# Kernel tuning notes

Hardware: AMD Instinct MI355X
Metric: run time of the kernel (lower is better)

Reference implementation:

```python
import jax, jax.numpy as jnp
import numpy as np

K = 3          # kernel_size
N = K * K      # sampling points per pixel
STRIDE = 1
PAD = 1
DIL = 1


def _conv2d(x, w, b):
    # standard NCHW conv for offset / modulation branches
    y = jax.lax.conv_general_dilated(
        x, w, window_strides=(STRIDE, STRIDE),
        padding=((PAD, PAD), (PAD, PAD)),
        rhs_dilation=(DIL, DIL),
        dimension_numbers=('NCHW', 'OIHW', 'NCHW'))
    return y + b[None, :, None, None]


def setup_inputs() -> dict:
    key = jax.random.key(0)
    ks = jax.random.split(key, 6)
    B, C, H, W, O = 8, 64, 96, 96, 64
    x = jax.random.normal(ks[0], (B, C, H, W), jnp.float32)
    # small random offset/modulation weights so sampling points are off-grid
    offset_w = jax.random.normal(ks[1], (2 * N, C, K, K), jnp.float32) * 0.01
    offset_b = jax.random.normal(ks[2], (2 * N,), jnp.float32) * 0.1
    m_w = jax.random.normal(ks[3], (N, C, K, K), jnp.float32) * 0.01
    m_b = jnp.zeros((N,), jnp.float32)
    # Conv3d(in=C, out=O, kernel=(1,1,N)) weight squeezed to [O, C, N]
    conv_w = jax.random.normal(ks[4], (O, C, N), jnp.float32) * (2.0 / (C * N)) ** 0.5
    conv_b = jnp.zeros((O,), jnp.float32)
    return dict(x=x, offset_w=offset_w, offset_b=offset_b,
                m_w=m_w, m_b=m_b, conv_w=conv_w, conv_b=conv_b)


def _deform_forward(x, offset_w, offset_b, m_w, m_b, conv_w, conv_b):
    B, C, H, W = x.shape
    offset = _conv2d(x, offset_w, offset_b)           # [B, 2n, h, w]
    m = jax.nn.sigmoid(_conv2d(x, m_w, m_b))          # [B, n, h, w]
    xp = jnp.pad(x, ((0, 0), (0, 0), (PAD, PAD), (PAD, PAD)))
    Hp, Wp = xp.shape[2], xp.shape[3]
    off = jnp.transpose(offset, (0, 2, 3, 1))         # [B, h, w, 2n]
    mod = jnp.transpose(m, (0, 2, 3, 1))              # [B, h, w, n]

    # p0: conv-center grid on the padded input; pn: kernel-tap offsets
    st = ((K - 1) // 2) * DIL
    p0_x = jnp.arange(st, Hp - (K // 2) * DIL, STRIDE, dtype=jnp.float32)  # [h]
    p0_y = jnp.arange(st, Wp - (K // 2) * DIL, STRIDE, dtype=jnp.float32)  # [w]
    r = jnp.arange(-((K - 1) // 2) * DIL, (K // 2) * DIL + 1, DIL, dtype=jnp.float32)
    pn_x, pn_y = jnp.meshgrid(r, r, indexing='ij')
    pn_x, pn_y = pn_x.reshape(N), pn_y.reshape(N)

    p_x = off[..., :N] + p0_x[None, :, None, None] + pn_x  # [B, h, w, n]
    p_y = off[..., N:] + p0_y[None, None, :, None] + pn_y

    fl_x = jnp.floor(jax.lax.stop_gradient(p_x))
    fl_y = jnp.floor(jax.lax.stop_gradient(p_y))
    q_tl_x = jnp.clip(fl_x, 0, Hp - 1).astype(jnp.int32)
    q_tl_y = jnp.clip(fl_y, 0, Wp - 1).astype(jnp.int32)
    q_br_x = jnp.clip(fl_x + 1, 0, Hp - 1).astype(jnp.int32)
    q_br_y = jnp.clip(fl_y + 1, 0, Wp - 1).astype(jnp.int32)

    pcx = jnp.clip(p_x, 0, Hp - 1)
    pcy = jnp.clip(p_y, 0, Wp - 1)

    tlx = q_tl_x.astype(pcx.dtype); tly = q_tl_y.astype(pcy.dtype)
    brx = q_br_x.astype(pcx.dtype); bry = q_br_y.astype(pcy.dtype)
    g_tl = (1 + (tlx - pcx)) * (1 + (tly - pcy))
    g_tr = (1 + (tlx - pcx)) * (1 - (bry - pcy))
    g_bl = (1 - (brx - pcx)) * (1 + (tly - pcy))
    g_br = (1 - (brx - pcx)) * (1 - (bry - pcy))

    xflat = xp.reshape(B, C, Hp * Wp)

    def gather(qx, qy):
        # per-batch gather: xf [C, Hp*Wp], idx [h, w, n] -> [C, h, w, n]
        return jax.vmap(lambda xf, i: xf[:, i])(xflat, qx * Wp + qy)

    xq_tl = gather(q_tl_x, q_tl_y)
    xq_tr = gather(q_tl_x, q_br_y)
    xq_bl = gather(q_br_x, q_tl_y)
    xq_br = gather(q_br_x, q_br_y)

    x_p = (g_tl[:, None] * xq_tl + g_tr[:, None] * xq_tr +
           g_bl[:, None] * xq_bl + g_br[:, None] * xq_br)
    x_p = x_p * mod[:, None]                           # modulation

    # Conv3d with (1,1,N) kernel == contraction over (C, N)
    out = jnp.einsum('bchwn,ocn->bohw', x_p, conv_w) + conv_b[None, :, None, None]
    return out


def reference(x, offset_w, offset_b, m_w, m_b, conv_w, conv_b):
    return _deform_forward(x, offset_w, offset_b, m_w, m_b, conv_w, conv_b)
```

## Files before the change

kernel.cpp:

```cpp
#include <hip/hip_runtime.h>
#include <hip/hip_fp16.h>
#include <cstddef>

#define B_   8
#define H_   96
#define W_   96
#define HW_  9216
#define PIX_ 73728

#define NWR    7
#define NWC    38
#define WINPX  266
#define NSLOTS 19

typedef __attribute__((ext_vector_type(8))) _Float16 halfx8;
typedef __attribute__((ext_vector_type(2))) __fp16 fp16x2_raw;
typedef __attribute__((ext_vector_type(4))) float floatx4;

#define XT_OFF   0
#define WFM_OFF  (XT_OFF + PIX_*64*2)
#define WFO_OFF  (WFM_OFF + 18*4*64*8*2)
#define WZ_OFF   (WFO_OFF + 18*2*64*8*2)

__device__ __forceinline__ unsigned pk2h(float a, float b) {
    fp16x2_raw h = __builtin_amdgcn_cvt_pkrtz(a, b);
    union { fp16x2_raw h2; unsigned u; } t; t.h2 = h; return t.u;
}
__device__ __forceinline__ halfx8 uph8(uint4 u) {
    union { uint4 u4; halfx8 h; } t; t.u4 = u; return t.h;
}
__device__ __forceinline__ halfx8 splat8(unsigned d) {
    union { unsigned u[4]; halfx8 h; } t;
    t.u[0] = d; t.u[1] = d; t.u[2] = d; t.u[3] = d; return t.h;
}
__device__ __forceinline__ void async_ld16(const void* g, void* l) {
    __builtin_amdgcn_global_load_lds((const __attribute__((address_space(1))) void*)g,
                                     (__attribute__((address_space(3))) void*)l,
                                     16, 0, 0);
}

__global__ __launch_bounds__(256) void k_transpose(const float* __restrict__ x,
                                                   unsigned short* __restrict__ xt,
                                                   const float* __restrict__ offw,
                                                   const float* __restrict__ mw,
                                                   const float* __restrict__ convw,
                                                   unsigned short* __restrict__ wfm,
                                                   unsigned short* __restrict__ wfo,
                                                   unsigned short* __restrict__ wz) {
    if (blockIdx.x >= 1152) {
        int g = (blockIdx.x - 1152) * 256 + threadIdx.x;
        if (g < 4608) {
            int lane = g & 63, mtks = g >> 6;
            int mt = mtks & 3, ks = mtks >> 2;
            int o = mt * 16 + (lane & 15), quad = lane >> 4;
            float v[8];
            #pragma unroll
            for (int j = 0; j < 8; ++j) {
                int k = ks * 32 + quad * 8 + j;
                int t = k / 64, c = k % 64;
                v[j] = convw[(size_t)(o * 64 + c) * 9 + t];
            }
            uint4 pk;
            pk.x = pk2h(v[0], v[1]); pk.y = pk2h(v[2], v[3]);
            pk.z = pk2h(v[4], v[5]); pk.w = pk2h(v[6], v[7]);
            *(uint4*)(wfm + (size_t)g * 8) = pk;
        } else if (g < 4608 + 2304) {
            int g2 = g - 4608;
            int lane = g2 & 63, mtks = g2 >> 6;
            int mt = mtks & 1, ks = mtks >> 1;
            int m = mt * 16 + (lane & 15), quad = lane >> 4;
            float v[8];
            #pragma unroll
            for (int j = 0; j < 8; ++j) {
                int k = ks * 32 + quad * 8 + j;
                int t = k / 64, c = k % 64;
                float f = 0.f;
                if (m < 18)      f = offw[(size_t)(m * 64 + c) * 9 + t];
                else if (m < 27) f = mw[(size_t)((m - 18) * 64 + c) * 9 + t];
                v[j] = f;
            }
            uint4 pk;
            pk.x = pk2h(v[0], v[1]); pk.y = pk2h(v[2], v[3]);
            pk.z = pk2h(v[4], v[5]); pk.w = pk2h(v[6], v[7]);
            *(uint4*)(wfo + (size_t)g2 * 8) = pk;
        } else if (g < 4608 + 2304 + 8) {
            uint4 z = make_uint4(0, 0, 0, 0);
            *(uint4*)(wz + (size_t)(g - 6912) * 8) = z;
        }
        return;
    }

    __shared__ float tile[64 * 65];
    int bb  = blockIdx.x / 144;
    int sp0 = (blockIdx.x % 144) * 64;
    int t = threadIdx.x;
    int s4 = (t & 15) * 4, cq = t >> 4;
    #pragma unroll
    for (int i = 0; i < 4; ++i) {
        int c = cq + 16 * i;
        float4 v = *(const float4*)&x[(size_t)(bb * 64 + c) * HW_ + sp0 + s4];
        tile[c * 65 + s4 + 0] = v.x;
        tile[c * 65 + s4 + 1] = v.y;
        tile[c * 65 + s4 + 2] = v.z;
        tile[c * 65 + s4 + 3] = v.w;
    }
    __syncthreads();
    int c8 = t & 7, sgrp = t >> 3;
    #pragma unroll
    for (int i = 0; i < 2; ++i) {
        int s2 = i * 32 + sgrp;
        uint4 pk;
        pk.x = pk2h(tile[(c8 * 8 + 0) * 65 + s2], tile[(c8 * 8 + 1) * 65 + s2]);
        pk.y = pk2h(tile[(c8 * 8 + 2) * 65 + s2], tile[(c8 * 8 + 3) * 65 + s2]);
        pk.z = pk2h(tile[(c8 * 8 + 4) * 65 + s2], tile[(c8 * 8 + 5) * 65 + s2]);
        pk.w = pk2h(tile[(c8 * 8 + 6) * 65 + s2], tile[(c8 * 8 + 7) * 65 + s2]);
        *(uint4*)(xt + (size_t)(bb * HW_ + sp0 + s2) * 64 + c8 * 8) = pk;
    }
}

__global__ __launch_bounds__(384, 4) void k_fused(const unsigned short* __restrict__ xt,
                                                  const unsigned short* __restrict__ wfo,
                                                  const unsigned short* __restrict__ wfm,
                                                  const float* __restrict__ offb,
                                                  const float* __restrict__ mb,
                                                  const float* __restrict__ convb,
                                                  const unsigned short* __restrict__ wz,
                                                  float* __restrict__ out) {
    __shared__ __align__(16) unsigned char s_win[(WINPX + NSLOTS) * 128];
    __shared__ __align__(16) unsigned char s_u[96 * 9 * 16];
    __shared__ int s_cnt;
    float* s_off = (float*)s_u;
    unsigned char* s_meta = s_u;

    int tid = threadIdx.x;
    int w = tid >> 6, lane = tid & 63, col = lane & 15, quad = lane >> 4;
    int blk = (blockIdx.x & 7) * 96 + (blockIdx.x >> 3);
    int bb  = blk / 96;
    int rem = blk % 96;
    int hr  = (rem / 3) * 3;
    int wc  = (rem % 3) * 32;
    const unsigned short* xtb = xt + (size_t)bb * HW_ * 64;

    if (tid == 0) s_cnt = 0;
    {
        int p0  = lane >> 3;
        int cgx = (lane & 7) ^ p0;
        const unsigned short* wzp = wz + cgx * 8;
        for (int i = w; i < 34; i += 6) {
            int p = i * 8 + p0;
            int wr = p / NWC, wcl = p - wr * NWC;
            int gr = hr - 2 + wr, gc = wc - 3 + wcl;
            bool ok = (p < WINPX) && ((unsigned)gr < 96u) && ((unsigned)gc < 96u);
            const unsigned short* src = ok ? (xtb + ((size_t)(gr * 96 + gc) * 64 + cgx * 8)) : wzp;
            async_ld16(src, s_win + i * 1024);
        }
    }
    __syncthreads();

    floatx4 aoff0 = (floatx4){0.f, 0.f, 0.f, 0.f};
    floatx4 aoff1 = (floatx4){0.f, 0.f, 0.f, 0.f};
    {
        int wr_base = 2 + (w >> 1);
        int wc_base = 3 + (w & 1) * 16 + col;
        #pragma unroll
        for (int t = 0; t < 9; ++t) {
            int dh = t / 3 - 1, dw = t % 3 - 1;
            int p = (wr_base + dh) * NWC + (wc_base + dw);
            int pb = p << 7, psw = (p & 7) << 4;
            #pragma unroll
            for (int ksl = 0; ksl < 2; ++ksl) {
                int ks = t * 2 + ksl;
                halfx8 a0 = *(const halfx8*)(wfo + ((size_t)(ks * 2 + 0) * 64 + lane) * 8);
                halfx8 a1 = *(const halfx8*)(wfo + ((size_t)(ks * 2 + 1) * 64 + lane) * 8);
                uint4 bvu = *(const uint4*)(s_win + pb + ((quad * 16 + ksl * 64) ^ psw));
                halfx8 bv = uph8(bvu);
                aoff0 = __builtin_amdgcn_mfma_f32_16x16x32_f16(a0, bv, aoff0, 0, 0, 0);
                aoff1 = __builtin_amdgcn_mfma_f32_16x16x32_f16(a1, bv, aoff1, 0, 0, 0);
            }
        }
    }
    #pragma unroll
    for (int r = 0; r < 4; ++r) {
        s_off[(quad * 4 + r) * 98 + (w * 16 + col)] = aoff0[r];
        int m = 16 + quad * 4 + r;
        if (m < 27) s_off[m * 98 + (w * 16 + col)] = aoff1[r];
    }
    __syncthreads();

    float ox0, oy0, mv0, ox1, oy1, mv1, ox2 = 0.f, oy2 = 0.f, mv2 = 0.f;
    bool has2 = tid < 96;
    {
        int px = tid % 96, n = tid / 96;
        ox0 = s_off[n * 98 + px]        + offb[n];
        oy0 = s_off[(9 + n) * 98 + px]  + offb[9 + n];
        mv0 = s_off[(18 + n) * 98 + px] + mb[n];
    }
    {
        int id = tid + 384;
        int px = id % 96, n = id / 96;
        ox1 = s_off[n * 98 + px]        + offb[n];
        oy1 = s_off[(9 + n) * 98 + px]  + offb[9 + n];
        mv1 = s_off[(18 + n) * 98 + px] + mb[n];
    }
    if (has2) {
        int id = tid + 768;
        int px = id % 96, n = id / 96;
        ox2 = s_off[n * 98 + px]        + offb[n];
        oy2 = s_off[(9 + n) * 98 + px]  + offb[9 + n];
        mv2 = s_off[(18 + n) * 98 + px] + mb[n];
    }
    __syncthreads();

    auto meta_one = [&](int id, float ox, float oy, float mv) {
        int px = id % 96, n = id / 96;
        float modv = 1.f / (1.f + __expf(-mv));
        int prow = hr + (px >> 5), pcol = wc + (px & 31);
        float pxx = ox + (float)(prow + 1) + (float)(n / 3 - 1);
        float pyy = oy + (float)(pcol + 1) + (float)(n % 3 - 1);
        float flx = floorf(pxx), fly = floorf(pyy);
        float tlxf = fminf(fmaxf(flx,       0.f), 97.f);
        float tlyf = fminf(fmaxf(fly,       0.f), 97.f);
        float brxf = fminf(fmaxf(flx + 1.f, 0.f), 97.f);
        float bryf = fminf(fmaxf(fly + 1.f, 0.f), 97.f);
        float pcx  = fminf(fmaxf(pxx, 0.f), 97.f);
        float pcy  = fminf(fmaxf(pyy, 0.f), 97.f);
        float gx0 = 1.f + tlxf - pcx;
        float gx1 = 1.f - (brxf - pcx);
        float gy0 = 1.f + tlyf - pcy;
        float gy1 = 1.f - (bryf - pcy);
        int tlx = (int)tlxf, tly = (int)tlyf, brx = (int)brxf, bry = (int)bryf;
        int   qxs[4] = {tlx, tlx, brx, brx};
        int   qys[4] = {tly, bry, tly, bry};
        float gs4[4] = {gx0 * gy0, gx0 * gy1, gx1 * gy0, gx1 * gy1};
        unsigned short si[4]; unsigned short hg[4];
        #pragma unroll
        for (int c4 = 0; c4 < 4; ++c4) {
            int qx = qxs[c4], qy = qys[c4];
            bool valid = (qx >= 1) && (qx <= 96) && (qy >= 1) && (qy <= 96);
            int gr = qx - 1, gc = qy - 1;
            int wr = gr - (hr - 2), wcl = gc - (wc - 3);
            bool inwin = ((unsigned)wr < (unsigned)NWR) && ((unsigned)wcl < (unsigned)NWC);
            unsigned short idxv; float gvf;
            if (inwin) {
                idxv = (unsigned short)(wr * NWC + wcl);
                gvf = gs4[c4] * modv;
            } else if (!valid) {
                idxv = 0; gvf = 0.f;
            } else {
                int s = atomicAdd(&s_cnt, 1);
                int gidx = gr * 96 + gc;
                if (s < NSLOTS) {
                    int ps = WINPX + s;
                    #pragma unroll
                    for (int ch = 0; ch < 8; ++ch) {
                        uint4 v = *(const uint4*)(xtb + (size_t)gidx * 64 + ch * 8);
                        *(uint4*)(s_win + (size_t)ps * 128 + ((ch ^ (ps & 7)) * 16)) = v;
                    }
                    idxv = (unsigned short)ps;
                } else {
                    idxv = (unsigned short)(0x8000u | (unsigned)gidx);
                }
                gvf = gs4[c4] * modv;
            }
            si[c4] = idxv;
            hg[c4] = __half_as_ushort(__float2half_rn(gvf));
        }
        uint4 mw4;
        mw4.x = si[0] | ((unsigned)si[1] << 16);
        mw4.y = si[2] | ((unsigned)si[3] << 16);
        mw4.z = hg[0] | ((unsigned)hg[1] << 16);
        mw4.w = hg[2] | ((unsigned)hg[3] << 16);
        *(uint4*)(s_meta + ((size_t)px * 9 + n) * 16) = mw4;
    };
    meta_one(tid,       ox0, oy0, mv0);
    meta_one(tid + 384, ox1, oy1, mv1);
    if (has2) meta_one(tid + 768, ox2, oy2, mv2);
    __syncthreads();

    int px3 = w * 16 + col;
    floatx4 acc[4];
    #pragma unroll
    for (int mt = 0; mt < 4; ++mt) acc[mt] = (floatx4){0.f, 0.f, 0.f, 0.f};

    int qk0 = quad * 16, qk1 = quad * 16 + 64;

    #pragma unroll
    for (int n = 0; n < 9; ++n) {
        uint4 mu = *(const uint4*)(s_meta + ((size_t)px3 * 9 + n) * 16);
        unsigned i0 = mu.x & 0xFFFFu, i1 = mu.x >> 16;
        unsigned i2 = mu.y & 0xFFFFu, i3 = mu.y >> 16;
        int pm0 = (i0 & 0x8000u) ? 0 : (int)i0;
        int pm1 = (i1 & 0x8000u) ? 0 : (int)i1;
        int pm2 = (i2 & 0x8000u) ? 0 : (int)i2;
        int pm3 = (i3 & 0x8000u) ? 0 : (int)i3;
        int b0 = pm0 << 7, s0 = (pm0 & 7) << 4;
        int b1 = pm1 << 7, s1 = (pm1 & 7) << 4;
        int b2 = pm2 << 7, s2 = (pm2 & 7) << 4;
        int b3 = pm3 << 7, s3 = (pm3 & 7) << 4;
        uint4 cA0 = *(const uint4*)(s_win + b0 + (qk0 ^ s0));
        uint4 cA1 = *(const uint4*)(s_win + b1 + (qk0 ^ s1));
        uint4 cA2 = *(const uint4*)(s_win + b2 + (qk0 ^ s2));
        uint4 cA3 = *(const uint4*)(s_win + b3 + (qk0 ^ s3));
        uint4 cB0 = *(const uint4*)(s_win + b0 + (qk1 ^ s0));
        uint4 cB1 = *(const uint4*)(s_win + b1 + (qk1 ^ s1));
        uint4 cB2 = *(const uint4*)(s_win + b2 + (qk1 ^ s2));
        uint4 cB3 = *(const uint4*)(s_win + b3 + (qk1 ^ s3));
        if (__any((int)((i0 | i1 | i2 | i3) & 0x8000u))) {
            if (i0 & 0x8000u) { size_t ga = (size_t)(i0 & 0x3FFFu) * 64 + quad * 8;
                cA0 = *(const uint4*)(xtb + ga); cB0 = *(const uint4*)(xtb + ga + 32); }
            if (i1 & 0x8000u) { size_t ga = (size_t)(i1 & 0x3FFFu) * 64 + quad * 8;
                cA1 = *(const uint4*)(xtb + ga); cB1 = *(const uint4*)(xtb + ga + 32); }
            if (i2 & 0x8000u) { size_t ga = (size_t)(i2 & 0x3FFFu) * 64 + quad * 8;
                cA2 = *(const uint4*)(xtb + ga); cB2 = *(const uint4*)(xtb + ga + 32); }
            if (i3 & 0x8000u) { size_t ga = (size_t)(i3 & 0x3FFFu) * 64 + quad * 8;
                cA3 = *(const uint4*)(xtb + ga); cB3 = *(const uint4*)(xtb + ga + 32); }
        }
        unsigned gl0 = (mu.z & 0xFFFFu) | (mu.z << 16);
        unsigned gl1 = (mu.z >> 16) | (mu.z & 0xFFFF0000u);
        unsigned gl2 = (mu.w & 0xFFFFu) | (mu.w << 16);
        unsigned gl3 = (mu.w >> 16) | (mu.w & 0xFFFF0000u);
        halfx8 g0 = splat8(gl0), g1 = splat8(gl1), g2 = splat8(gl2), g3 = splat8(gl3);
        halfx8 vA = uph8(cA0) * g0;
        vA += uph8(cA1) * g1; vA += uph8(cA2) * g2; vA += uph8(cA3) * g3;
        halfx8 vB = uph8(cB0) * g0;
        vB += uph8(cB1) * g1; vB += uph8(cB2) * g2; vB += uph8(cB3) * g3;
        #pragma unroll
        for (int mt = 0; mt < 4; ++mt) {
            halfx8 afA = *(const halfx8*)(wfm + ((size_t)((n * 2 + 0) * 4 + mt) * 64 + lane) * 8);
            halfx8 afB = *(const halfx8*)(wfm + ((size_t)((n * 2 + 1) * 4 + mt) * 64 + lane) * 8);
            acc[mt] = __builtin_amdgcn_mfma_f32_16x16x32_f16(afA, vA, acc[mt], 0, 0, 0);
            acc[mt] = __builtin_amdgcn_mfma_f32_16x16x32_f16(afB, vB, acc[mt], 0, 0, 0);
        }
    }

    int sp = (hr + (w >> 1)) * 96 + wc + (w & 1) * 16 + col;
    #pragma unroll
    for (int mt = 0; mt < 4; ++mt) {
        float4 cb4 = *(const float4*)&convb[mt * 16 + quad * 4];
        #pragma unroll
        for (int r = 0; r < 4; ++r) {
            int o = mt * 16 + quad * 4 + r;
            float bias = (r == 0) ? cb4.x : (r == 1) ? cb4.y : (r == 2) ? cb4.z : cb4.w;
            out[(size_t)(bb * 64 + o) * HW_ + sp] = acc[mt][r] + bias;
        }
    }
}

extern "C" void kernel_launch(void* const* d_in, const int* in_sizes, int n_in,
                              void* d_out, int out_size, void* d_ws, size_t ws_size,
                              hipStream_t stream) {
    const float* x     = (const float*)d_in[0];
    const float* offw  = (const float*)d_in[1];
    const float* offb  = (const float*)d_in[2];
    const float* mw    = (const float*)d_in[3];
    const float* mb    = (const float*)d_in[4];
    const float* convw = (const float*)d_in[5];
    const float* convb = (const float*)d_in[6];
    char* ws = (char*)d_ws;
    unsigned short* xt16 = (unsigned short*)(ws + XT_OFF);
    unsigned short* wfm  = (unsigned short*)(ws + WFM_OFF);
    unsigned short* wfo  = (unsigned short*)(ws + WFO_OFF);
    unsigned short* wz   = (unsigned short*)(ws + WZ_OFF);
    float* out = (float*)d_out;

    k_transpose<<<dim3(1152 + 28), dim3(256), 0, stream>>>(x, xt16, offw, mw, convw, wfm, wfo, wz);
    k_fused    <<<dim3(768),       dim3(384), 0, stream>>>(xt16, wfo, wfm, offb, mb, convb, wz, out);
}
```

Measured before the change: 109.3 us.

## Fuse transpose and deform kernels into one cooperative launch with grid sync

```diff
diff --git a/kernel.cpp b/kernel.cpp
--- a/kernel.cpp
+++ b/kernel.cpp
@@ -1,6 +1,9 @@
 #include <hip/hip_runtime.h>
 #include <hip/hip_fp16.h>
+#include <hip/hip_cooperative_groups.h>
 #include <cstddef>
+
+namespace cg = cooperative_groups;
 
 #define B_   8
 #define H_   96
@@ -39,109 +42,64 @@
                                      16, 0, 0);
 }
 
-__global__ __launch_bounds__(256) void k_transpose(const float* __restrict__ x,
-                                                   unsigned short* __restrict__ xt,
-                                                   const float* __restrict__ offw,
-                                                   const float* __restrict__ mw,
-                                                   const float* __restrict__ convw,
-                                                   unsigned short* __restrict__ wfm,
-                                                   unsigned short* __restrict__ wfo,
-                                                   unsigned short* __restrict__ wz) {
-    if (blockIdx.x >= 1152) {
-        int g = (blockIdx.x - 1152) * 256 + threadIdx.x;
-        if (g < 4608) {
-            int lane = g & 63, mtks = g >> 6;
-            int mt = mtks & 3, ks = mtks >> 2;
-            int o = mt * 16 + (lane & 15), quad = lane >> 4;
-            float v[8];
-            #pragma unroll
-            for (int j = 0; j < 8; ++j) {
-                int k = ks * 32 + quad * 8 + j;
-                int t = k / 64, c = k % 64;
-                v[j] = convw[(size_t)(o * 64 + c) * 9 + t];
-            }
-            uint4 pk;
-            pk.x = pk2h(v[0], v[1]); pk.y = pk2h(v[2], v[3]);
-            pk.z = pk2h(v[4], v[5]); pk.w = pk2h(v[6], v[7]);
-            *(uint4*)(wfm + (size_t)g * 8) = pk;
-        } else if (g < 4608 + 2304) {
-            int g2 = g - 4608;
-            int lane = g2 & 63, mtks = g2 >> 6;
-            int mt = mtks & 1, ks = mtks >> 1;
-            int m = mt * 16 + (lane & 15), quad = lane >> 4;
-            float v[8];
-            #pragma unroll
-            for (int j = 0; j < 8; ++j) {
-                int k = ks * 32 + quad * 8 + j;
-                int t = k / 64, c = k % 64;
-                float f = 0.f;
-                if (m < 18)      f = offw[(size_t)(m * 64 + c) * 9 + t];
-                else if (m < 27) f = mw[(size_t)((m - 18) * 64 + c) * 9 + t];
-                v[j] = f;
-            }
-            uint4 pk;
-            pk.x = pk2h(v[0], v[1]); pk.y = pk2h(v[2], v[3]);
-            pk.z = pk2h(v[4], v[5]); pk.w = pk2h(v[6], v[7]);
-            *(uint4*)(wfo + (size_t)g2 * 8) = pk;
-        } else if (g < 4608 + 2304 + 8) {
-            uint4 z = make_uint4(0, 0, 0, 0);
-            *(uint4*)(wz + (size_t)(g - 6912) * 8) = z;
-        }
-        return;
-    }
-
-    __shared__ float tile[64 * 65];
-    int bb  = blockIdx.x / 144;
-    int sp0 = (blockIdx.x % 144) * 64;
-    int t = threadIdx.x;
-    int s4 = (t & 15) * 4, cq = t >> 4;
-    #pragma unroll
-    for (int i = 0; i < 4; ++i) {
-        int c = cq + 16 * i;
-        float4 v = *(const float4*)&x[(size_t)(bb * 64 + c) * HW_ + sp0 + s4];
-        tile[c * 65 + s4 + 0] = v.x;
-        tile[c * 65 + s4 + 1] = v.y;
-        tile[c * 65 + s4 + 2] = v.z;
-        tile[c * 65 + s4 + 3] = v.w;
-    }
-    __syncthreads();
-    int c8 = t & 7, sgrp = t >> 3;
-    #pragma unroll
-    for (int i = 0; i < 2; ++i) {
-        int s2 = i * 32 + sgrp;
+__device__ __forceinline__ void prep_weight_item(int g,
+                                                 const float* __restrict__ offw,
+                                                 const float* __restrict__ mw,
+                                                 const float* __restrict__ convw,
+                                                 unsigned short* __restrict__ wfm,
+                                                 unsigned short* __restrict__ wfo) {
+    if (g < 4608) {
+        int lane = g & 63, mtks = g >> 6;
+        int mt = mtks & 3, ks = mtks >> 2;
+        int o = mt * 16 + (lane & 15), quad = lane >> 4;
+        float v[8];
+        #pragma unroll
+        for (int j = 0; j < 8; ++j) {
+            int k = ks * 32 + quad * 8 + j;
+            int t = k / 64, c = k % 64;
+            v[j] = convw[(size_t)(o * 64 + c) * 9 + t];
+        }
         uint4 pk;
-        pk.x = pk2h(tile[(c8 * 8 + 0) * 65 + s2], tile[(c8 * 8 + 1) * 65 + s2]);
-        pk.y = pk2h(tile[(c8 * 8 + 2) * 65 + s2], tile[(c8 * 8 + 3) * 65 + s2]);
-        pk.z = pk2h(tile[(c8 * 8 + 4) * 65 + s2], tile[(c8 * 8 + 5) * 65 + s2]);
-        pk.w = pk2h(tile[(c8 * 8 + 6) * 65 + s2], tile[(c8 * 8 + 7) * 65 + s2]);
-        *(uint4*)(xt + (size_t)(bb * HW_ + sp0 + s2) * 64 + c8 * 8) = pk;
-    }
-}
-
-__global__ __launch_bounds__(384, 4) void k_fused(const unsigned short* __restrict__ xt,
-                                                  const unsigned short* __restrict__ wfo,
-                                                  const unsigned short* __restrict__ wfm,
-                                                  const float* __restrict__ offb,
-                                                  const float* __restrict__ mb,
-                                                  const float* __restrict__ convb,
-                                                  const unsigned short* __restrict__ wz,
-                                                  float* __restrict__ out) {
-    __shared__ __align__(16) unsigned char s_win[(WINPX + NSLOTS) * 128];
-    __shared__ __align__(16) unsigned char s_u[96 * 9 * 16];
-    __shared__ int s_cnt;
+        pk.x = pk2h(v[0], v[1]); pk.y = pk2h(v[2], v[3]);
+        pk.z = pk2h(v[4], v[5]); pk.w = pk2h(v[6], v[7]);
+        *(uint4*)(wfm + (size_t)g * 8) = pk;
+    } else if (g < 4608 + 2304) {
+        int g2 = g - 4608;
+        int lane = g2 & 63, mtks = g2 >> 6;
+        int mt = mtks & 1, ks = mtks >> 1;
+        int m = mt * 16 + (lane & 15), quad = lane >> 4;
+        float v[8];
+        #pragma unroll
+        for (int j = 0; j < 8; ++j) {
+            int k = ks * 32 + quad * 8 + j;
+            int t = k / 64, c = k % 64;
+            float f = 0.f;
+            if (m < 18)      f = offw[(size_t)(m * 64 + c) * 9 + t];
+            else if (m < 27) f = mw[(size_t)((m - 18) * 64 + c) * 9 + t];
+            v[j] = f;
+        }
+        uint4 pk;
+        pk.x = pk2h(v[0], v[1]); pk.y = pk2h(v[2], v[3]);
+        pk.z = pk2h(v[4], v[5]); pk.w = pk2h(v[6], v[7]);
+        *(uint4*)(wfo + (size_t)g2 * 8) = pk;
+    }
+}
+
+__device__ __forceinline__ void deform_body(unsigned char* s_win, unsigned char* s_u,
+                                            int* s_cnt_p,
+                                            int tid, int bb, int hr, int wc,
+                                            const unsigned short* __restrict__ xtb,
+                                            const unsigned short* __restrict__ wfo,
+                                            const unsigned short* __restrict__ wfm,
+                                            const float* __restrict__ offb,
+                                            const float* __restrict__ mb,
+                                            const float* __restrict__ convb,
+                                            const unsigned short* __restrict__ wz,
+                                            float* __restrict__ out) {
     float* s_off = (float*)s_u;
     unsigned char* s_meta = s_u;
-
-    int tid = threadIdx.x;
     int w = tid >> 6, lane = tid & 63, col = lane & 15, quad = lane >> 4;
-    int blk = (blockIdx.x & 7) * 96 + (blockIdx.x >> 3);
-    int bb  = blk / 96;
-    int rem = blk % 96;
-    int hr  = (rem / 3) * 3;
-    int wc  = (rem % 3) * 32;
-    const unsigned short* xtb = xt + (size_t)bb * HW_ * 64;
-
-    if (tid == 0) s_cnt = 0;
+
     {
         int p0  = lane >> 3;
         int cgx = (lane & 7) ^ p0;
@@ -247,7 +205,7 @@
             } else if (!valid) {
                 idxv = 0; gvf = 0.f;
             } else {
-                int s = atomicAdd(&s_cnt, 1);
+                int s = atomicAdd(s_cnt_p, 1);
                 int gidx = gr * 96 + gc;
                 if (s < NSLOTS) {
                     int ps = WINPX + s;
@@ -346,6 +304,137 @@
     }
 }
 
+__global__ __launch_bounds__(384, 5) void k_all(const float* __restrict__ x,
+                                                unsigned short* __restrict__ xt,
+                                                const float* __restrict__ offw,
+                                                const float* __restrict__ mw,
+                                                const float* __restrict__ convw,
+                                                unsigned short* __restrict__ wfm,
+                                                unsigned short* __restrict__ wfo,
+                                                const float* __restrict__ offb,
+                                                const float* __restrict__ mb,
+                                                const float* __restrict__ convb,
+                                                unsigned short* __restrict__ wz,
+                                                float* __restrict__ out) {
+    __shared__ __align__(16) unsigned char s_win[(WINPX + NSLOTS) * 128];
+    __shared__ __align__(16) unsigned char s_u[96 * 9 * 16];
+    __shared__ int s_cnt;
+
+    cg::grid_group grid = cg::this_grid();
+    int tid = threadIdx.x;
+    int blk = (blockIdx.x & 7) * 96 + (blockIdx.x >> 3);
+    int bb  = blk / 96;
+    int rem = blk % 96;
+    int hr  = (rem / 3) * 3;
+    int wc  = (rem % 3) * 32;
+    const unsigned short* xtb = xt + (size_t)bb * HW_ * 64;
+    if (tid == 0) s_cnt = 0;
+
+    {
+        float* tf = (float*)s_win;
+        #pragma unroll
+        for (int it = 0; it < 4; ++it) {
+            int task = it * 384 + tid;
+            int o = task * 4;
+            int c = o / 96, p = o - c * 96;
+            int pr = p >> 5, pc = p & 31;
+            float4 v = *(const float4*)&x[(size_t)(bb * 64 + c) * HW_ + (hr + pr) * 96 + wc + pc];
+            tf[c * 97 + p + 0] = v.x;
+            tf[c * 97 + p + 1] = v.y;
+            tf[c * 97 + p + 2] = v.z;
+            tf[c * 97 + p + 3] = v.w;
+        }
+        if (blockIdx.x < 18) prep_weight_item(blockIdx.x * 384 + tid, offw, mw, convw, wfm, wfo);
+        if (blockIdx.x == 18 && tid < 8) {
+            uint4 z = make_uint4(0, 0, 0, 0);
+            *(uint4*)(wz + (size_t)tid * 8) = z;
+        }
+        __syncthreads();
+        #pragma unroll
+        for (int it = 0; it < 2; ++it) {
+            int task = it * 384 + tid;
+            int px = task >> 3, cgp = task & 7;
+            uint4 pk;
+            pk.x = pk2h(tf[(cgp * 8 + 0) * 97 + px], tf[(cgp * 8 + 1) * 97 + px]);
+            pk.y = pk2h(tf[(cgp * 8 + 2) * 97 + px], tf[(cgp * 8 + 3) * 97 + px]);
+            pk.z = pk2h(tf[(cgp * 8 + 4) * 97 + px], tf[(cgp * 8 + 5) * 97 + px]);
+            pk.w = pk2h(tf[(cgp * 8 + 6) * 97 + px], tf[(cgp * 8 + 7) * 97 + px]);
+            *(uint4*)(xt + ((size_t)(bb * HW_ + (hr + (px >> 5)) * 96 + wc + (px & 31))) * 64 + cgp * 8) = pk;
+        }
+    }
+    grid.sync();
+
+    deform_body(s_win, s_u, &s_cnt, tid, bb, hr, wc, xtb, wfo, wfm, offb, mb, convb, wz, out);
+}
+
+__global__ __launch_bounds__(256) void k_transpose(const float* __restrict__ x,
+                                                   unsigned short* __restrict__ xt,
+                                                   const float* __restrict__ offw,
+                                                   const float* __restrict__ mw,
+                                                   const float* __restrict__ convw,
+                                                   unsigned short* __restrict__ wfm,
+                                                   unsigned short* __restrict__ wfo,
+                                                   unsigned short* __restrict__ wz) {
+    if (blockIdx.x >= 1152) {
+        int g = (blockIdx.x - 1152) * 256 + threadIdx.x;
+        if (g < 6912) prep_weight_item(g, offw, mw, convw, wfm, wfo);
+        else if (g < 6920) {
+            uint4 z = make_uint4(0, 0, 0, 0);
+            *(uint4*)(wz + (size_t)(g - 6912) * 8) = z;
+        }
+        return;
+    }
+    __shared__ float tile[64 * 65];
+    int bb  = blockIdx.x / 144;
+    int sp0 = (blockIdx.x % 144) * 64;
+    int t = threadIdx.x;
+    int s4 = (t & 15) * 4, cq = t >> 4;
+    #pragma unroll
+    for (int i = 0; i < 4; ++i) {
+        int c = cq + 16 * i;
+        float4 v = *(const float4*)&x[(size_t)(bb * 64 + c) * HW_ + sp0 + s4];
+        tile[c * 65 + s4 + 0] = v.x;
+        tile[c * 65 + s4 + 1] = v.y;
+        tile[c * 65 + s4 + 2] = v.z;
+        tile[c * 65 + s4 + 3] = v.w;
+    }
+    __syncthreads();
+    int c8 = t & 7, sgrp = t >> 3;
+    #pragma unroll
+    for (int i = 0; i < 2; ++i) {
+        int s2 = i * 32 + sgrp;
+        uint4 pk;
+        pk.x = pk2h(tile[(c8 * 8 + 0) * 65 + s2], tile[(c8 * 8 + 1) * 65 + s2]);
+        pk.y = pk2h(tile[(c8 * 8 + 2) * 65 + s2], tile[(c8 * 8 + 3) * 65 + s2]);
+        pk.z = pk2h(tile[(c8 * 8 + 4) * 65 + s2], tile[(c8 * 8 + 5) * 65 + s2]);
+        pk.w = pk2h(tile[(c8 * 8 + 6) * 65 + s2], tile[(c8 * 8 + 7) * 65 + s2]);
+        *(uint4*)(xt + (size_t)(bb * HW_ + sp0 + s2) * 64 + c8 * 8) = pk;
+    }
+}
+
+__global__ __launch_bounds__(384, 5) void k_fused(const unsigned short* __restrict__ xt,
+                                                  const unsigned short* __restrict__ wfo,
+                                                  const unsigned short* __restrict__ wfm,
+                                                  const float* __restrict__ offb,
+                                                  const float* __restrict__ mb,
+                                                  const float* __restrict__ convb,
+                                                  const unsigned short* __restrict__ wz,
+                                                  float* __restrict__ out) {
+    __shared__ __align__(16) unsigned char s_win[(WINPX + NSLOTS) * 128];
+    __shared__ __align__(16) unsigned char s_u[96 * 9 * 16];
+    __shared__ int s_cnt;
+    int tid = threadIdx.x;
+    int blk = (blockIdx.x & 7) * 96 + (blockIdx.x >> 3);
+    int bb  = blk / 96;
+    int rem = blk % 96;
+    int hr  = (rem / 3) * 3;
+    int wc  = (rem % 3) * 32;
+    const unsigned short* xtb = xt + (size_t)bb * HW_ * 64;
+    if (tid == 0) s_cnt = 0;
+    __syncthreads();
+    deform_body(s_win, s_u, &s_cnt, tid, bb, hr, wc, xtb, wfo, wfm, offb, mb, convb, wz, out);
+}
+
 extern "C" void kernel_launch(void* const* d_in, const int* in_sizes, int n_in,
                               void* d_out, int out_size, void* d_ws, size_t ws_size,
                               hipStream_t stream) {
@@ -363,6 +452,12 @@
     unsigned short* wz   = (unsigned short*)(ws + WZ_OFF);
     float* out = (float*)d_out;
 
-    k_transpose<<<dim3(1152 + 28), dim3(256), 0, stream>>>(x, xt16, offw, mw, convw, wfm, wfo, wz);
-    k_fused    <<<dim3(768),       dim3(384), 0, stream>>>(xt16, wfo, wfm, offb, mb, convb, wz, out);
-}
+    void* args[] = {(void*)&x, (void*)&xt16, (void*)&offw, (void*)&mw, (void*)&convw,
+                    (void*)&wfm, (void*)&wfo, (void*)&offb, (void*)&mb, (void*)&convb,
+                    (void*)&wz, (void*)&out};
+    hipError_t e = hipLaunchCooperativeKernel((void*)k_all, dim3(768), dim3(384), args, 0, stream);
+    if (e != hipSuccess) {
+        k_transpose<<<dim3(1152 + 28), dim3(256), 0, stream>>>(x, xt16, offw, mw, convw, wfm, wfo, wz);
+        k_fused    <<<dim3(768),       dim3(384), 0, stream>>>(xt16, wfo, wfm, offb, mb, convb, wz, out);
+    }
+}
```

New measurement: 218.6 us. +100.1%, slower.
